# Optimization experiments

Hardware: AMD Instinct MI355X
Metric: run time of the kernel (lower is better)

## Reference

```python
import jax, jax.numpy as jnp
import numpy as np


def fake_quant(w, bits):
    # Symmetric per-tensor fake quantization with straight-through estimator.
    qmax = 2.0 ** (bits - 1) - 1.0
    scale = jnp.max(jnp.abs(w)) / qmax
    wq = jnp.clip(jnp.round(w / scale), -qmax, qmax) * scale
    return w + jax.lax.stop_gradient(wq - w)


def setup_inputs() -> dict:
    key = jax.random.key(0)
    k = jax.random.split(key, 5)
    B, S, D, H = 64, 196, 768, 3072
    x = jax.random.normal(k[0], (B, S, D), dtype=jnp.float32)
    w1 = jax.random.normal(k[1], (H, D), dtype=jnp.float32) * (1.0 / np.sqrt(D))
    b1 = jax.random.normal(k[2], (H,), dtype=jnp.float32) * 0.01
    w2 = jax.random.normal(k[3], (D, H), dtype=jnp.float32) * (1.0 / np.sqrt(H))
    b2 = jax.random.normal(k[4], (D,), dtype=jnp.float32) * 0.01
    return {"x": x, "w1": w1, "b1": b1, "w2": w2, "b2": b2, "bits": 8}


def reference(x, w1, b1, w2, b2, bits):
    # fc1 (fake-quant weight) -> ReLU -> fc2 (fake-quant weight)
    w1q = fake_quant(w1, bits)
    w2q = fake_quant(w2, bits)
    h = jnp.einsum('bsd,hd->bsh', x, w1q) + b1   # [B,S,3072]
    h = jax.nn.relu(h)
    out = jnp.einsum('bsh,dh->bsd', h, w2q) + b2  # [B,S,768]
    return out
```

## Files before the change

### kernel.cpp

```cpp
#include <hip/hip_runtime.h>
#include <hip/hip_bf16.h>
#include <stdint.h>

typedef __attribute__((ext_vector_type(8))) short bf16x8;
typedef __attribute__((ext_vector_type(4))) float f32x4;

__device__ __forceinline__ unsigned short f2bf(float f) {
  __hip_bfloat16 h = __float2bfloat16(f);
  return *reinterpret_cast<unsigned short*>(&h);
}

__global__ void absmax2_kernel(const float* __restrict__ w1, const float* __restrict__ w2,
                               int n4, unsigned int* __restrict__ out) {
  const float* w = blockIdx.y ? w2 : w1;
  __shared__ unsigned int red[256];
  unsigned int m = 0u;
  const uint4* w4 = reinterpret_cast<const uint4*>(w);
  for (int i = blockIdx.x * blockDim.x + threadIdx.x; i < n4;
       i += gridDim.x * blockDim.x) {
    uint4 v = w4[i];
    m = max(m, v.x & 0x7fffffffu);
    m = max(m, v.y & 0x7fffffffu);
    m = max(m, v.z & 0x7fffffffu);
    m = max(m, v.w & 0x7fffffffu);
  }
  red[threadIdx.x] = m;
  __syncthreads();
  for (int s = 128; s > 0; s >>= 1) {
    if ((int)threadIdx.x < s)
      red[threadIdx.x] = max(red[threadIdx.x], red[threadIdx.x + s]);
    __syncthreads();
  }
  if (threadIdx.x == 0) atomicMax(out + blockIdx.y, red[0]);
}

__global__ void quantcast_kernel(const float* __restrict__ w1, const float* __restrict__ w2,
                                 const float* __restrict__ x,
                                 int n4w, int n4x,
                                 const unsigned int* __restrict__ maxbits,
                                 const int* __restrict__ bits,
                                 unsigned short* __restrict__ o1,
                                 unsigned short* __restrict__ o2,
                                 unsigned short* __restrict__ ox) {
  if (blockIdx.y == 2) {
    const float4* x4 = reinterpret_cast<const float4*>(x);
    ushort4* o4 = reinterpret_cast<ushort4*>(ox);
    for (int i = blockIdx.x * blockDim.x + threadIdx.x; i < n4x;
         i += gridDim.x * blockDim.x) {
      float4 v = x4[i];
      o4[i] = make_ushort4(f2bf(v.x), f2bf(v.y), f2bf(v.z), f2bf(v.w));
    }
    return;
  }
  const float* w = blockIdx.y ? w2 : w1;
  unsigned short* o = blockIdx.y ? o2 : o1;
  const float qmax = (float)((1 << (*bits - 1)) - 1);
  const float scale = __uint_as_float(maxbits[blockIdx.y]) / qmax;
  const float4* w4 = reinterpret_cast<const float4*>(w);
  ushort4* o4 = reinterpret_cast<ushort4*>(o);
  for (int i = blockIdx.x * blockDim.x + threadIdx.x; i < n4w;
       i += gridDim.x * blockDim.x) {
    float4 v = w4[i];
    float a = fminf(fmaxf(rintf(v.x / scale), -qmax), qmax) * scale;
    float b = fminf(fmaxf(rintf(v.y / scale), -qmax), qmax) * scale;
    float c = fminf(fmaxf(rintf(v.z / scale), -qmax), qmax) * scale;
    float d = fminf(fmaxf(rintf(v.w / scale), -qmax), qmax) * scale;
    o4[i] = make_ushort4(f2bf(a), f2bf(b), f2bf(c), f2bf(d));
  }
}

template<bool RELU, bool BF16_OUT>
__global__ __launch_bounds__(512, 2)
void gemm8w(const unsigned short* __restrict__ A,
            const unsigned short* __restrict__ B,
            const float* __restrict__ bias,
            void* __restrict__ Cout,
            int M, int N, int K, int gx) {
  extern __shared__ unsigned short lds[];

  const int nwg = gridDim.x;
  const int orig = blockIdx.x;
  const int q = nwg >> 3, r = nwg & 7;
  const int xcd = orig & 7, cidx = orig >> 3;
  const int wgid = (xcd < r ? xcd * (q + 1) : r * (q + 1) + (xcd - r) * q) + cidx;
  const int bx = wgid % gx;
  const int by = wgid / gx;

  const int tid = threadIdx.x;
  const int lane = tid & 63;
  const int wave = tid >> 6;
  const int wr = wave >> 2;
  const int wc = wave & 3;
  const long brow = (long)by * 256;
  const long bcol = (long)bx * 256;

  f32x4 acc[8][4] = {};

  const int fr = lane & 15;
  const int fq = lane >> 4;
  const int swz8 = ((lane & 3) ^ ((lane >> 3) & 3)) * 8;
  const int sgrow = wave * 16 + (lane >> 2);

  auto SA = [&](int t, int kh) {
    unsigned short* dst = lds + ((t & 1) * 2 + kh) * 8192 + wave * 16 * 32;
    const unsigned short* g = A + (brow + sgrow) * (long)K + t * 64 + kh * 32 + swz8;
#pragma unroll
    for (int c = 0; c < 2; ++c)
      __builtin_amdgcn_global_load_lds(
          (const __attribute__((address_space(1))) void*)(g + (long)c * 128 * K),
          (__attribute__((address_space(3))) void*)(dst + c * 128 * 32), 16, 0, 0);
  };
  auto SB = [&](int t, int kh) {
    unsigned short* dst = lds + 32768 + ((t & 1) * 2 + kh) * 8192 + wave * 16 * 32;
    const unsigned short* g = B + (bcol + sgrow) * (long)K + t * 64 + kh * 32 + swz8;
#pragma unroll
    for (int c = 0; c < 2; ++c)
      __builtin_amdgcn_global_load_lds(
          (const __attribute__((address_space(1))) void*)(g + (long)c * 128 * K),
          (__attribute__((address_space(3))) void*)(dst + c * 128 * 32), 16, 0, 0);
  };

  auto RDA = [&](int b, int ks, int mseg, bf16x8* a) {
    const unsigned short* base = lds + (b * 2 + ks) * 8192;
#pragma unroll
    for (int mi = 0; mi < 4; ++mi) {
      const int row = wr * 128 + mseg * 64 + mi * 16 + fr;
      a[mi] = *reinterpret_cast<const bf16x8*>(base + row * 32 + ((fq ^ ((row >> 1) & 3)) * 8));
    }
  };
  auto RDB = [&](int b, int ks, bf16x8* bb) {
    const unsigned short* base = lds + 32768 + (b * 2 + ks) * 8192;
#pragma unroll
    for (int ni = 0; ni < 4; ++ni) {
      const int row = wc * 64 + ni * 16 + fr;
      bb[ni] = *reinterpret_cast<const bf16x8*>(base + row * 32 + ((fq ^ ((row >> 1) & 3)) * 8));
    }
  };
  auto MM = [&](int mseg, bf16x8* a, bf16x8* bb) {
#pragma unroll
    for (int mi = 0; mi < 4; ++mi)
#pragma unroll
      for (int ni = 0; ni < 4; ++ni)
        acc[mseg * 4 + mi][ni] = __builtin_amdgcn_mfma_f32_16x16x32_bf16(
            a[mi], bb[ni], acc[mseg * 4 + mi][ni], 0, 0, 0);
  };

  const int nt = K / 64;
  SA(0, 0); SB(0, 0); SA(0, 1); SB(0, 1); SA(1, 0); SB(1, 0);

  bf16x8 a[4], bb[4];
  for (int t = 0; t < nt; ++t) {
    const int b = t & 1;
    if (t + 1 < nt) {
      SA(t + 1, 1);
      asm volatile("s_waitcnt vmcnt(10)" ::: "memory");
    } else {
      asm volatile("s_waitcnt vmcnt(4)" ::: "memory");
    }
    asm volatile("s_barrier" ::: "memory");
    RDA(b, 0, 0, a); RDB(b, 0, bb);
    asm volatile("s_waitcnt lgkmcnt(0)" ::: "memory");
    __builtin_amdgcn_sched_barrier(0);
    __builtin_amdgcn_s_setprio(1);
    MM(0, a, bb);
    __builtin_amdgcn_s_setprio(0);
    asm volatile("s_barrier" ::: "memory");
    if (t + 1 < nt) SB(t + 1, 1);
    RDA(b, 0, 1, a);
    asm volatile("s_waitcnt lgkmcnt(0)" ::: "memory");
    __builtin_amdgcn_sched_barrier(0);
    __builtin_amdgcn_s_setprio(1);
    MM(1, a, bb);
    __builtin_amdgcn_s_setprio(0);
    asm volatile("s_barrier" ::: "memory");
    if (t + 2 < nt) SA(t + 2, 0);
    if (t + 3 <= nt)      asm volatile("s_waitcnt vmcnt(10)" ::: "memory");
    else if (t == nt - 2) asm volatile("s_waitcnt vmcnt(8)"  ::: "memory");
    else                  asm volatile("s_waitcnt vmcnt(0)"  ::: "memory");
    asm volatile("s_barrier" ::: "memory");
    RDA(b, 1, 0, a); RDB(b, 1, bb);
    asm volatile("s_waitcnt lgkmcnt(0)" ::: "memory");
    __builtin_amdgcn_sched_barrier(0);
    __builtin_amdgcn_s_setprio(1);
    MM(0, a, bb);
    __builtin_amdgcn_s_setprio(0);
    asm volatile("s_barrier" ::: "memory");
    if (t + 2 < nt) SB(t + 2, 0);
    RDA(b, 1, 1, a);
    asm volatile("s_waitcnt lgkmcnt(0)" ::: "memory");
    __builtin_amdgcn_sched_barrier(0);
    __builtin_amdgcn_s_setprio(1);
    MM(1, a, bb);
    __builtin_amdgcn_s_setprio(0);
    asm volatile("s_barrier" ::: "memory");
  }

#pragma unroll
  for (int ni = 0; ni < 4; ++ni) {
    const long col = bcol + wc * 64 + ni * 16 + fr;
    const float bv = bias[col];
#pragma unroll
    for (int mi = 0; mi < 8; ++mi) {
#pragma unroll
      for (int rr = 0; rr < 4; ++rr) {
        const long row = brow + wr * 128 + mi * 16 + fq * 4 + rr;
        float v = acc[mi][ni][rr] + bv;
        if (RELU) v = fmaxf(v, 0.0f);
        if (BF16_OUT)
          ((unsigned short*)Cout)[row * N + col] = f2bf(v);
        else
          ((float*)Cout)[row * N + col] = v;
      }
    }
  }
}

extern "C" void kernel_launch(void* const* d_in, const int* in_sizes, int n_in,
                              void* d_out, int out_size, void* d_ws, size_t ws_size,
                              hipStream_t stream) {
  const float* x  = (const float*)d_in[0];
  const float* w1 = (const float*)d_in[1];
  const float* b1 = (const float*)d_in[2];
  const float* w2 = (const float*)d_in[3];
  const float* b2 = (const float*)d_in[4];
  const int* bits = (const int*)d_in[5];

  const int M = 64 * 196;
  const int D = 768, H = 3072;
  const int nx = M * D;
  const int nw1 = H * D;

  char* ws = (char*)d_ws;
  unsigned int* scales = (unsigned int*)ws;
  unsigned short* xb  = (unsigned short*)(ws + 256);
  unsigned short* w1q = (unsigned short*)(ws + 256 + (size_t)nx * 2);
  unsigned short* w2q = (unsigned short*)(ws + 256 + (size_t)nx * 2 + (size_t)nw1 * 2);
  unsigned short* hb  = (unsigned short*)(ws + 256 + (size_t)nx * 2 + (size_t)nw1 * 4);

  static bool attr_done = false;
  if (!attr_done) {
    hipFuncSetAttribute((const void*)gemm8w<true, true>,
                        hipFuncAttributeMaxDynamicSharedMemorySize, 131072);
    hipFuncSetAttribute((const void*)gemm8w<false, false>,
                        hipFuncAttributeMaxDynamicSharedMemorySize, 131072);
    attr_done = true;
  }

  hipMemsetAsync(scales, 0, 8, stream);
  absmax2_kernel<<<dim3(512, 2), 256, 0, stream>>>(w1, w2, nw1 / 4, scales);
  quantcast_kernel<<<dim3(768, 3), 256, 0, stream>>>(w1, w2, x, nw1 / 4, nx / 4,
                                                     scales, bits, w1q, w2q, xb);

  gemm8w<true, true><<<(M / 256) * (H / 256), 512, 131072, stream>>>(
      xb, w1q, b1, hb, M, H, D, H / 256);
  gemm8w<false, false><<<(M / 256) * (D / 256), 512, 131072, stream>>>(
      hb, w2q, b2, d_out, M, D, H, D / 256);
}
```

Measured before the change: 208.5 us.

## Use BK=32 static-LDS GEMM for fc1 and fuse absmax with x cast

Adds a GEMM variant with a K-step of 32 and statically allocated LDS (64KB) for the first layer, which has a short K=768. Smaller LDS allows more resident workgroups or fewer pipeline fill costs. The second layer keeps the BK=64 pipeline. The x bf16 cast is moved into the absmax kernel so it runs alongside the reduction, and the weight quantization runs as a separate kernel. The shallower prefetch in the BK=32 path may expose more memory latency.

```diff
diff --git a/kernel.cpp b/kernel.cpp
--- a/kernel.cpp
+++ b/kernel.cpp
@@ -10,38 +10,10 @@
   return *reinterpret_cast<unsigned short*>(&h);
 }
 
-__global__ void absmax2_kernel(const float* __restrict__ w1, const float* __restrict__ w2,
-                               int n4, unsigned int* __restrict__ out) {
-  const float* w = blockIdx.y ? w2 : w1;
-  __shared__ unsigned int red[256];
-  unsigned int m = 0u;
-  const uint4* w4 = reinterpret_cast<const uint4*>(w);
-  for (int i = blockIdx.x * blockDim.x + threadIdx.x; i < n4;
-       i += gridDim.x * blockDim.x) {
-    uint4 v = w4[i];
-    m = max(m, v.x & 0x7fffffffu);
-    m = max(m, v.y & 0x7fffffffu);
-    m = max(m, v.z & 0x7fffffffu);
-    m = max(m, v.w & 0x7fffffffu);
-  }
-  red[threadIdx.x] = m;
-  __syncthreads();
-  for (int s = 128; s > 0; s >>= 1) {
-    if ((int)threadIdx.x < s)
-      red[threadIdx.x] = max(red[threadIdx.x], red[threadIdx.x + s]);
-    __syncthreads();
-  }
-  if (threadIdx.x == 0) atomicMax(out + blockIdx.y, red[0]);
-}
-
-__global__ void quantcast_kernel(const float* __restrict__ w1, const float* __restrict__ w2,
-                                 const float* __restrict__ x,
-                                 int n4w, int n4x,
-                                 const unsigned int* __restrict__ maxbits,
-                                 const int* __restrict__ bits,
-                                 unsigned short* __restrict__ o1,
-                                 unsigned short* __restrict__ o2,
-                                 unsigned short* __restrict__ ox) {
+__global__ void prep_kernel(const float* __restrict__ w1, const float* __restrict__ w2,
+                            const float* __restrict__ x, int n4w, int n4x,
+                            unsigned int* __restrict__ out_scales,
+                            unsigned short* __restrict__ ox) {
   if (blockIdx.y == 2) {
     const float4* x4 = reinterpret_cast<const float4*>(x);
     ushort4* o4 = reinterpret_cast<ushort4*>(ox);
@@ -53,12 +25,38 @@
     return;
   }
   const float* w = blockIdx.y ? w2 : w1;
+  __shared__ unsigned int red[256];
+  unsigned int m = 0u;
+  const uint4* w4 = reinterpret_cast<const uint4*>(w);
+  for (int i = blockIdx.x * blockDim.x + threadIdx.x; i < n4w;
+       i += gridDim.x * blockDim.x) {
+    uint4 v = w4[i];
+    m = max(m, v.x & 0x7fffffffu);
+    m = max(m, v.y & 0x7fffffffu);
+    m = max(m, v.z & 0x7fffffffu);
+    m = max(m, v.w & 0x7fffffffu);
+  }
+  red[threadIdx.x] = m;
+  __syncthreads();
+  for (int s = 128; s > 0; s >>= 1) {
+    if ((int)threadIdx.x < s)
+      red[threadIdx.x] = max(red[threadIdx.x], red[threadIdx.x + s]);
+    __syncthreads();
+  }
+  if (threadIdx.x == 0) atomicMax(out_scales + blockIdx.y, red[0]);
+}
+
+__global__ void quant2_kernel(const float* __restrict__ w1, const float* __restrict__ w2,
+                              int n4, const unsigned int* __restrict__ maxbits,
+                              const int* __restrict__ bits,
+                              unsigned short* __restrict__ o1, unsigned short* __restrict__ o2) {
+  const float* w = blockIdx.y ? w2 : w1;
   unsigned short* o = blockIdx.y ? o2 : o1;
   const float qmax = (float)((1 << (*bits - 1)) - 1);
   const float scale = __uint_as_float(maxbits[blockIdx.y]) / qmax;
   const float4* w4 = reinterpret_cast<const float4*>(w);
   ushort4* o4 = reinterpret_cast<ushort4*>(o);
-  for (int i = blockIdx.x * blockDim.x + threadIdx.x; i < n4w;
+  for (int i = blockIdx.x * blockDim.x + threadIdx.x; i < n4;
        i += gridDim.x * blockDim.x) {
     float4 v = w4[i];
     float a = fminf(fmaxf(rintf(v.x / scale), -qmax), qmax) * scale;
@@ -69,14 +67,16 @@
   }
 }
 
+
 template<bool RELU, bool BF16_OUT>
 __global__ __launch_bounds__(512, 2)
-void gemm8w(const unsigned short* __restrict__ A,
-            const unsigned short* __restrict__ B,
-            const float* __restrict__ bias,
-            void* __restrict__ Cout,
-            int M, int N, int K, int gx) {
-  extern __shared__ unsigned short lds[];
+void gemm8w32(const unsigned short* __restrict__ A,
+              const unsigned short* __restrict__ B,
+              const float* __restrict__ bias,
+              void* __restrict__ Cout,
+              int M, int N, int K, int gx) {
+  __shared__ __attribute__((aligned(16))) unsigned short Abuf[2][256 * 32];
+  __shared__ __attribute__((aligned(16))) unsigned short Bbuf[2][256 * 32];
 
   const int nwg = gridDim.x;
   const int orig = blockIdx.x;
@@ -101,35 +101,34 @@
   const int swz8 = ((lane & 3) ^ ((lane >> 3) & 3)) * 8;
   const int sgrow = wave * 16 + (lane >> 2);
 
-  auto SA = [&](int t, int kh) {
-    unsigned short* dst = lds + ((t & 1) * 2 + kh) * 8192 + wave * 16 * 32;
-    const unsigned short* g = A + (brow + sgrow) * (long)K + t * 64 + kh * 32 + swz8;
+  auto SA = [&](int tt) {
+    unsigned short* dst = &Abuf[tt & 1][wave * 16 * 32];
+    const unsigned short* g = A + (brow + sgrow) * (long)K + tt * 32 + swz8;
 #pragma unroll
     for (int c = 0; c < 2; ++c)
       __builtin_amdgcn_global_load_lds(
           (const __attribute__((address_space(1))) void*)(g + (long)c * 128 * K),
           (__attribute__((address_space(3))) void*)(dst + c * 128 * 32), 16, 0, 0);
   };
-  auto SB = [&](int t, int kh) {
-    unsigned short* dst = lds + 32768 + ((t & 1) * 2 + kh) * 8192 + wave * 16 * 32;
-    const unsigned short* g = B + (bcol + sgrow) * (long)K + t * 64 + kh * 32 + swz8;
+  auto SB = [&](int tt) {
+    unsigned short* dst = &Bbuf[tt & 1][wave * 16 * 32];
+    const unsigned short* g = B + (bcol + sgrow) * (long)K + tt * 32 + swz8;
 #pragma unroll
     for (int c = 0; c < 2; ++c)
       __builtin_amdgcn_global_load_lds(
           (const __attribute__((address_space(1))) void*)(g + (long)c * 128 * K),
           (__attribute__((address_space(3))) void*)(dst + c * 128 * 32), 16, 0, 0);
   };
-
-  auto RDA = [&](int b, int ks, int mseg, bf16x8* a) {
-    const unsigned short* base = lds + (b * 2 + ks) * 8192;
+  auto RDA = [&](int b, int mseg, bf16x8* a) {
+    const unsigned short* base = &Abuf[b][0];
 #pragma unroll
     for (int mi = 0; mi < 4; ++mi) {
       const int row = wr * 128 + mseg * 64 + mi * 16 + fr;
       a[mi] = *reinterpret_cast<const bf16x8*>(base + row * 32 + ((fq ^ ((row >> 1) & 3)) * 8));
     }
   };
-  auto RDB = [&](int b, int ks, bf16x8* bb) {
-    const unsigned short* base = lds + 32768 + (b * 2 + ks) * 8192;
+  auto RDB = [&](int b, bf16x8* bb) {
+    const unsigned short* base = &Bbuf[b][0];
 #pragma unroll
     for (int ni = 0; ni < 4; ++ni) {
       const int row = wc * 64 + ni * 16 + fr;
@@ -145,48 +144,28 @@
             a[mi], bb[ni], acc[mseg * 4 + mi][ni], 0, 0, 0);
   };
 
-  const int nt = K / 64;
-  SA(0, 0); SB(0, 0); SA(0, 1); SB(0, 1); SA(1, 0); SB(1, 0);
+  const int nt = K / 32;
+  SA(0); SB(0);
 
   bf16x8 a[4], bb[4];
   for (int t = 0; t < nt; ++t) {
     const int b = t & 1;
     if (t + 1 < nt) {
-      SA(t + 1, 1);
-      asm volatile("s_waitcnt vmcnt(10)" ::: "memory");
+      SA(t + 1);
+      asm volatile("s_waitcnt vmcnt(2)" ::: "memory");
     } else {
-      asm volatile("s_waitcnt vmcnt(4)" ::: "memory");
-    }
-    asm volatile("s_barrier" ::: "memory");
-    RDA(b, 0, 0, a); RDB(b, 0, bb);
+      asm volatile("s_waitcnt vmcnt(0)" ::: "memory");
+    }
+    asm volatile("s_barrier" ::: "memory");
+    RDA(b, 0, a); RDB(b, bb);
     asm volatile("s_waitcnt lgkmcnt(0)" ::: "memory");
     __builtin_amdgcn_sched_barrier(0);
     __builtin_amdgcn_s_setprio(1);
     MM(0, a, bb);
     __builtin_amdgcn_s_setprio(0);
     asm volatile("s_barrier" ::: "memory");
-    if (t + 1 < nt) SB(t + 1, 1);
-    RDA(b, 0, 1, a);
-    asm volatile("s_waitcnt lgkmcnt(0)" ::: "memory");
-    __builtin_amdgcn_sched_barrier(0);
-    __builtin_amdgcn_s_setprio(1);
-    MM(1, a, bb);
-    __builtin_amdgcn_s_setprio(0);
-    asm volatile("s_barrier" ::: "memory");
-    if (t + 2 < nt) SA(t + 2, 0);
-    if (t + 3 <= nt)      asm volatile("s_waitcnt vmcnt(10)" ::: "memory");
-    else if (t == nt - 2) asm volatile("s_waitcnt vmcnt(8)"  ::: "memory");
-    else                  asm volatile("s_waitcnt vmcnt(0)"  ::: "memory");
-    asm volatile("s_barrier" ::: "memory");
-    RDA(b, 1, 0, a); RDB(b, 1, bb);
-    asm volatile("s_waitcnt lgkmcnt(0)" ::: "memory");
-    __builtin_amdgcn_sched_barrier(0);
-    __builtin_amdgcn_s_setprio(1);
-    MM(0, a, bb);
-    __builtin_amdgcn_s_setprio(0);
-    asm volatile("s_barrier" ::: "memory");
-    if (t + 2 < nt) SB(t + 2, 0);
-    RDA(b, 1, 1, a);
+    if (t + 1 < nt) SB(t + 1);
+    RDA(b, 1, a);
     asm volatile("s_waitcnt lgkmcnt(0)" ::: "memory");
     __builtin_amdgcn_sched_barrier(0);
     __builtin_amdgcn_s_setprio(1);
@@ -215,6 +194,149 @@
   }
 }
 
+template<bool RELU, bool BF16_OUT>
+__global__ __launch_bounds__(512, 2)
+void gemm8w64(const unsigned short* __restrict__ A, const unsigned short* __restrict__ B,
+              const float* __restrict__ bias, void* __restrict__ Cout,
+              int M, int N, int K, int gx) {
+  extern __shared__ unsigned short lds[];
+
+  const int nwg = gridDim.x;
+  const int orig = blockIdx.x;
+  const int q = nwg >> 3, r = nwg & 7;
+  const int xcd = orig & 7, cidx = orig >> 3;
+  const int wgid = (xcd < r ? xcd * (q + 1) : r * (q + 1) + (xcd - r) * q) + cidx;
+  const int bx = wgid % gx;
+  const int by = wgid / gx;
+
+  const int tid = threadIdx.x;
+  const int lane = tid & 63;
+  const int wave = tid >> 6;
+  const int wr = wave >> 2;
+  const int wc = wave & 3;
+  const long brow = (long)by * 256;
+  const long bcol = (long)bx * 256;
+
+  f32x4 acc[8][4] = {};
+
+  const int fr = lane & 15;
+  const int fq = lane >> 4;
+  const int swz8 = ((lane & 3) ^ ((lane >> 3) & 3)) * 8;
+  const int sgrow = wave * 16 + (lane >> 2);
+
+  auto SA = [&](int t, int kh) {
+    unsigned short* dst = lds + ((t & 1) * 2 + kh) * 8192 + wave * 16 * 32;
+    const unsigned short* g = A + (brow + sgrow) * (long)K + t * 64 + kh * 32 + swz8;
+#pragma unroll
+    for (int c = 0; c < 2; ++c)
+      __builtin_amdgcn_global_load_lds(
+          (const __attribute__((address_space(1))) void*)(g + (long)c * 128 * K),
+          (__attribute__((address_space(3))) void*)(dst + c * 128 * 32), 16, 0, 0);
+  };
+  auto SB = [&](int t, int kh) {
+    unsigned short* dst = lds + 32768 + ((t & 1) * 2 + kh) * 8192 + wave * 16 * 32;
+    const unsigned short* g = B + (bcol + sgrow) * (long)K + t * 64 + kh * 32 + swz8;
+#pragma unroll
+    for (int c = 0; c < 2; ++c)
+      __builtin_amdgcn_global_load_lds(
+          (const __attribute__((address_space(1))) void*)(g + (long)c * 128 * K),
+          (__attribute__((address_space(3))) void*)(dst + c * 128 * 32), 16, 0, 0);
+  };
+  auto RDA = [&](int b, int ks, int mseg, bf16x8* a) {
+    const unsigned short* base = lds + (b * 2 + ks) * 8192;
+#pragma unroll
+    for (int mi = 0; mi < 4; ++mi) {
+      const int row = wr * 128 + mseg * 64 + mi * 16 + fr;
+      a[mi] = *reinterpret_cast<const bf16x8*>(base + row * 32 + ((fq ^ ((row >> 1) & 3)) * 8));
+    }
+  };
+  auto RDB = [&](int b, int ks, bf16x8* bb) {
+    const unsigned short* base = lds + 32768 + (b * 2 + ks) * 8192;
+#pragma unroll
+    for (int ni = 0; ni < 4; ++ni) {
+      const int row = wc * 64 + ni * 16 + fr;
+      bb[ni] = *reinterpret_cast<const bf16x8*>(base + row * 32 + ((fq ^ ((row >> 1) & 3)) * 8));
+    }
+  };
+  auto MM = [&](int mseg, bf16x8* a, bf16x8* bb) {
+#pragma unroll
+    for (int mi = 0; mi < 4; ++mi)
+#pragma unroll
+      for (int ni = 0; ni < 4; ++ni)
+        acc[mseg * 4 + mi][ni] = __builtin_amdgcn_mfma_f32_16x16x32_bf16(
+            a[mi], bb[ni], acc[mseg * 4 + mi][ni], 0, 0, 0);
+  };
+
+  const int nt = K / 64;
+  SA(0, 0); SB(0, 0); SA(0, 1); SB(0, 1); SA(1, 0); SB(1, 0);
+
+  bf16x8 a[4], bb[4];
+  for (int t = 0; t < nt; ++t) {
+    const int b = t & 1;
+    if (t + 1 < nt) {
+      SA(t + 1, 1);
+      asm volatile("s_waitcnt vmcnt(10)" ::: "memory");
+    } else {
+      asm volatile("s_waitcnt vmcnt(4)" ::: "memory");
+    }
+    asm volatile("s_barrier" ::: "memory");
+    RDA(b, 0, 0, a); RDB(b, 0, bb);
+    asm volatile("s_waitcnt lgkmcnt(0)" ::: "memory");
+    __builtin_amdgcn_sched_barrier(0);
+    __builtin_amdgcn_s_setprio(1);
+    MM(0, a, bb);
+    __builtin_amdgcn_s_setprio(0);
+    asm volatile("s_barrier" ::: "memory");
+    if (t + 1 < nt) SB(t + 1, 1);
+    RDA(b, 0, 1, a);
+    asm volatile("s_waitcnt lgkmcnt(0)" ::: "memory");
+    __builtin_amdgcn_sched_barrier(0);
+    __builtin_amdgcn_s_setprio(1);
+    MM(1, a, bb);
+    __builtin_amdgcn_s_setprio(0);
+    asm volatile("s_barrier" ::: "memory");
+    if (t + 2 < nt) SA(t + 2, 0);
+    if (t + 3 <= nt)      asm volatile("s_waitcnt vmcnt(10)" ::: "memory");
+    else if (t == nt - 2) asm volatile("s_waitcnt vmcnt(8)"  ::: "memory");
+    else                  asm volatile("s_waitcnt vmcnt(0)"  ::: "memory");
+    asm volatile("s_barrier" ::: "memory");
+    RDA(b, 1, 0, a); RDB(b, 1, bb);
+    asm volatile("s_waitcnt lgkmcnt(0)" ::: "memory");
+    __builtin_amdgcn_sched_barrier(0);
+    __builtin_amdgcn_s_setprio(1);
+    MM(0, a, bb);
+    __builtin_amdgcn_s_setprio(0);
+    asm volatile("s_barrier" ::: "memory");
+    if (t + 2 < nt) SB(t + 2, 0);
+    RDA(b, 1, 1, a);
+    asm volatile("s_waitcnt lgkmcnt(0)" ::: "memory");
+    __builtin_amdgcn_sched_barrier(0);
+    __builtin_amdgcn_s_setprio(1);
+    MM(1, a, bb);
+    __builtin_amdgcn_s_setprio(0);
+    asm volatile("s_barrier" ::: "memory");
+  }
+
+#pragma unroll
+  for (int ni = 0; ni < 4; ++ni) {
+    const long col = bcol + wc * 64 + ni * 16 + fr;
+    const float bv = bias[col];
+#pragma unroll
+    for (int mi = 0; mi < 8; ++mi) {
+#pragma unroll
+      for (int rr = 0; rr < 4; ++rr) {
+        const long row = brow + wr * 128 + mi * 16 + fq * 4 + rr;
+        float v = acc[mi][ni][rr] + bv;
+        if (RELU) v = fmaxf(v, 0.0f);
+        if (BF16_OUT)
+          ((unsigned short*)Cout)[row * N + col] = f2bf(v);
+        else
+          ((float*)Cout)[row * N + col] = v;
+      }
+    }
+  }
+}
+
 extern "C" void kernel_launch(void* const* d_in, const int* in_sizes, int n_in,
                               void* d_out, int out_size, void* d_ws, size_t ws_size,
                               hipStream_t stream) {
@@ -237,22 +359,15 @@
   unsigned short* w2q = (unsigned short*)(ws + 256 + (size_t)nx * 2 + (size_t)nw1 * 2);
   unsigned short* hb  = (unsigned short*)(ws + 256 + (size_t)nx * 2 + (size_t)nw1 * 4);
 
-  static bool attr_done = false;
-  if (!attr_done) {
-    hipFuncSetAttribute((const void*)gemm8w<true, true>,
-                        hipFuncAttributeMaxDynamicSharedMemorySize, 131072);
-    hipFuncSetAttribute((const void*)gemm8w<false, false>,
-                        hipFuncAttributeMaxDynamicSharedMemorySize, 131072);
-    attr_done = true;
-  }
+  hipFuncSetAttribute((const void*)gemm8w64<false, false>,
+                      hipFuncAttributeMaxDynamicSharedMemorySize, 131072);
 
   hipMemsetAsync(scales, 0, 8, stream);
-  absmax2_kernel<<<dim3(512, 2), 256, 0, stream>>>(w1, w2, nw1 / 4, scales);
-  quantcast_kernel<<<dim3(768, 3), 256, 0, stream>>>(w1, w2, x, nw1 / 4, nx / 4,
-                                                     scales, bits, w1q, w2q, xb);
-
-  gemm8w<true, true><<<(M / 256) * (H / 256), 512, 131072, stream>>>(
+  prep_kernel<<<dim3(512, 3), 256, 0, stream>>>(w1, w2, x, nw1 / 4, nx / 4, scales, xb);
+  quant2_kernel<<<dim3(512, 2), 256, 0, stream>>>(w1, w2, nw1 / 4, scales, bits, w1q, w2q);
+
+  gemm8w32<true, true><<<(M / 256) * (H / 256), 512, 0, stream>>>(
       xb, w1q, b1, hb, M, H, D, H / 256);
-  gemm8w<false, false><<<(M / 256) * (D / 256), 512, 131072, stream>>>(
+  gemm8w64<false, false><<<(M / 256) * (D / 256), 512, 131072, stream>>>(
       hb, w2q, b2, d_out, M, D, H, D / 256);
 }
```

Measured after the change: 222.2 us. 6.6% more time.

## Use 128x128 tile GEMM for fc1 and fold x cast into absmax pass

Applied to the files above, without the earlier changes.

Replaces the 256x256, 8-wave GEMM for the first layer (K=768) with a new 128x128-tile, 4-wave kernel. It uses static LDS, a BK=64 XOR swizzle and double-buffered global_load_lds staging. The x-to-bf16 cast now runs in the same launch as the weight absmax reduction, and weight quantization moves to a separate kernel, so the x cast no longer waits on the reduction. The smaller tiles give more workgroups for the short-K GEMM, which should help load balance and latency hiding, at the cost of lower data reuse per tile. The second GEMM keeps the old kernel under a new name, and the one-time attribute guard is dropped, so the attribute is now set on every call.

```diff
diff --git a/kernel.cpp b/kernel.cpp
--- a/kernel.cpp
+++ b/kernel.cpp
@@ -10,38 +10,10 @@
   return *reinterpret_cast<unsigned short*>(&h);
 }
 
-__global__ void absmax2_kernel(const float* __restrict__ w1, const float* __restrict__ w2,
-                               int n4, unsigned int* __restrict__ out) {
-  const float* w = blockIdx.y ? w2 : w1;
-  __shared__ unsigned int red[256];
-  unsigned int m = 0u;
-  const uint4* w4 = reinterpret_cast<const uint4*>(w);
-  for (int i = blockIdx.x * blockDim.x + threadIdx.x; i < n4;
-       i += gridDim.x * blockDim.x) {
-    uint4 v = w4[i];
-    m = max(m, v.x & 0x7fffffffu);
-    m = max(m, v.y & 0x7fffffffu);
-    m = max(m, v.z & 0x7fffffffu);
-    m = max(m, v.w & 0x7fffffffu);
-  }
-  red[threadIdx.x] = m;
-  __syncthreads();
-  for (int s = 128; s > 0; s >>= 1) {
-    if ((int)threadIdx.x < s)
-      red[threadIdx.x] = max(red[threadIdx.x], red[threadIdx.x + s]);
-    __syncthreads();
-  }
-  if (threadIdx.x == 0) atomicMax(out + blockIdx.y, red[0]);
-}
-
-__global__ void quantcast_kernel(const float* __restrict__ w1, const float* __restrict__ w2,
-                                 const float* __restrict__ x,
-                                 int n4w, int n4x,
-                                 const unsigned int* __restrict__ maxbits,
-                                 const int* __restrict__ bits,
-                                 unsigned short* __restrict__ o1,
-                                 unsigned short* __restrict__ o2,
-                                 unsigned short* __restrict__ ox) {
+__global__ void prep_kernel(const float* __restrict__ w1, const float* __restrict__ w2,
+                            const float* __restrict__ x, int n4w, int n4x,
+                            unsigned int* __restrict__ out_scales,
+                            unsigned short* __restrict__ ox) {
   if (blockIdx.y == 2) {
     const float4* x4 = reinterpret_cast<const float4*>(x);
     ushort4* o4 = reinterpret_cast<ushort4*>(ox);
@@ -53,12 +25,38 @@
     return;
   }
   const float* w = blockIdx.y ? w2 : w1;
+  __shared__ unsigned int red[256];
+  unsigned int m = 0u;
+  const uint4* w4 = reinterpret_cast<const uint4*>(w);
+  for (int i = blockIdx.x * blockDim.x + threadIdx.x; i < n4w;
+       i += gridDim.x * blockDim.x) {
+    uint4 v = w4[i];
+    m = max(m, v.x & 0x7fffffffu);
+    m = max(m, v.y & 0x7fffffffu);
+    m = max(m, v.z & 0x7fffffffu);
+    m = max(m, v.w & 0x7fffffffu);
+  }
+  red[threadIdx.x] = m;
+  __syncthreads();
+  for (int s = 128; s > 0; s >>= 1) {
+    if ((int)threadIdx.x < s)
+      red[threadIdx.x] = max(red[threadIdx.x], red[threadIdx.x + s]);
+    __syncthreads();
+  }
+  if (threadIdx.x == 0) atomicMax(out_scales + blockIdx.y, red[0]);
+}
+
+__global__ void quant2_kernel(const float* __restrict__ w1, const float* __restrict__ w2,
+                              int n4, const unsigned int* __restrict__ maxbits,
+                              const int* __restrict__ bits,
+                              unsigned short* __restrict__ o1, unsigned short* __restrict__ o2) {
+  const float* w = blockIdx.y ? w2 : w1;
   unsigned short* o = blockIdx.y ? o2 : o1;
   const float qmax = (float)((1 << (*bits - 1)) - 1);
   const float scale = __uint_as_float(maxbits[blockIdx.y]) / qmax;
   const float4* w4 = reinterpret_cast<const float4*>(w);
   ushort4* o4 = reinterpret_cast<ushort4*>(o);
-  for (int i = blockIdx.x * blockDim.x + threadIdx.x; i < n4w;
+  for (int i = blockIdx.x * blockDim.x + threadIdx.x; i < n4;
        i += gridDim.x * blockDim.x) {
     float4 v = w4[i];
     float a = fminf(fmaxf(rintf(v.x / scale), -qmax), qmax) * scale;
@@ -70,13 +68,15 @@
 }
 
 template<bool RELU, bool BF16_OUT>
-__global__ __launch_bounds__(512, 2)
-void gemm8w(const unsigned short* __restrict__ A,
-            const unsigned short* __restrict__ B,
-            const float* __restrict__ bias,
-            void* __restrict__ Cout,
-            int M, int N, int K, int gx) {
-  extern __shared__ unsigned short lds[];
+__global__ __launch_bounds__(256)
+void gemm1_bt(const unsigned short* __restrict__ A,
+              const unsigned short* __restrict__ B,
+              const float* __restrict__ bias,
+              void* __restrict__ Cout,
+              int M, int N, int K, int gx) {
+  constexpr int BK = 64, MF = 4;
+  __shared__ __attribute__((aligned(16))) unsigned short As[2][128 * BK];
+  __shared__ __attribute__((aligned(16))) unsigned short Bs[2][128 * BK];
 
   const int nwg = gridDim.x;
   const int orig = blockIdx.x;
@@ -89,6 +89,125 @@
   const int tid = threadIdx.x;
   const int lane = tid & 63;
   const int wave = tid >> 6;
+  const int wr = wave >> 1;
+  const int wc = wave & 1;
+  const long brow = (long)by * 128;
+  const long bcol = (long)bx * 128;
+
+  f32x4 acc[MF][4] = {};
+
+  const int srow = lane >> 3;
+  const int gslot = ((lane & 7) ^ (lane >> 3)) * 8;
+  const int fr = lane & 15;
+  const int fs = lane >> 4;
+
+  auto stage = [&](int k0, int b) {
+#pragma unroll
+    for (int it = 0; it < 4; ++it) {
+      const int c = it * 4 + wave;
+      const unsigned short* ga = A + (brow + c * 8 + srow) * (long)K + k0 + gslot;
+      __builtin_amdgcn_global_load_lds(
+          (const __attribute__((address_space(1))) void*)ga,
+          (__attribute__((address_space(3))) void*)(&As[b][c * 512]), 16, 0, 0);
+    }
+#pragma unroll
+    for (int it = 0; it < 4; ++it) {
+      const int c = it * 4 + wave;
+      const unsigned short* gb = B + (bcol + c * 8 + srow) * (long)K + k0 + gslot;
+      __builtin_amdgcn_global_load_lds(
+          (const __attribute__((address_space(1))) void*)gb,
+          (__attribute__((address_space(3))) void*)(&Bs[b][c * 512]), 16, 0, 0);
+    }
+  };
+
+  const int nt = K / BK;
+  stage(0, 0);
+  stage(BK, 1);
+
+  for (int t = 0; t < nt; ++t) {
+    const int b = t & 1;
+    if (t < nt - 1) asm volatile("s_waitcnt vmcnt(8)" ::: "memory");
+    else            asm volatile("s_waitcnt vmcnt(0)" ::: "memory");
+    __builtin_amdgcn_s_barrier();
+
+    const unsigned short* as = &As[b][0];
+    const unsigned short* bs = &Bs[b][0];
+#pragma unroll
+    for (int kk = 0; kk < 2; ++kk) {
+      const int s = kk * 4 + fs;
+      bf16x8 a[MF], bb[4];
+#pragma unroll
+      for (int m = 0; m < MF; ++m) {
+        const int row = wr * 64 + m * 16 + fr;
+        a[m] = *reinterpret_cast<const bf16x8*>(as + row * BK + ((s ^ (row & 7)) * 8));
+      }
+#pragma unroll
+      for (int n = 0; n < 4; ++n) {
+        const int row = wc * 64 + n * 16 + fr;
+        bb[n] = *reinterpret_cast<const bf16x8*>(bs + row * BK + ((s ^ (row & 7)) * 8));
+      }
+#pragma unroll
+      for (int m = 0; m < MF; ++m)
+#pragma unroll
+        for (int n = 0; n < 4; ++n)
+          acc[m][n] = __builtin_amdgcn_mfma_f32_16x16x32_bf16(bb[n], a[m], acc[m][n], 0, 0, 0);
+    }
+
+    asm volatile("s_waitcnt lgkmcnt(0)" ::: "memory");
+    __builtin_amdgcn_sched_barrier(0);
+    __builtin_amdgcn_s_barrier();
+    if (t + 2 < nt) stage((t + 2) * BK, b);
+  }
+
+  const int colq = fs * 4;
+  float4 bv[4];
+#pragma unroll
+  for (int n = 0; n < 4; ++n)
+    bv[n] = *reinterpret_cast<const float4*>(&bias[bcol + wc * 64 + n * 16 + colq]);
+#pragma unroll
+  for (int m = 0; m < MF; ++m) {
+    const long row = brow + wr * 64 + m * 16 + fr;
+#pragma unroll
+    for (int n = 0; n < 4; ++n) {
+      const long cb = bcol + wc * 64 + n * 16 + colq;
+      float v0 = acc[m][n][0] + bv[n].x;
+      float v1 = acc[m][n][1] + bv[n].y;
+      float v2 = acc[m][n][2] + bv[n].z;
+      float v3 = acc[m][n][3] + bv[n].w;
+      if (RELU) {
+        v0 = fmaxf(v0, 0.0f); v1 = fmaxf(v1, 0.0f);
+        v2 = fmaxf(v2, 0.0f); v3 = fmaxf(v3, 0.0f);
+      }
+      if (BF16_OUT) {
+        uint2 o;
+        o.x = (unsigned int)f2bf(v0) | ((unsigned int)f2bf(v1) << 16);
+        o.y = (unsigned int)f2bf(v2) | ((unsigned int)f2bf(v3) << 16);
+        *reinterpret_cast<uint2*>((unsigned short*)Cout + row * N + cb) = o;
+      } else {
+        *reinterpret_cast<float4*>((float*)Cout + row * N + cb) = make_float4(v0, v1, v2, v3);
+      }
+    }
+  }
+}
+
+template<bool RELU, bool BF16_OUT>
+__global__ __launch_bounds__(512, 2)
+void gemm8w64(const unsigned short* __restrict__ A, const unsigned short* __restrict__ B,
+              const float* __restrict__ bias, void* __restrict__ Cout,
+              int M, int N, int K, int gx) {
+  extern __shared__ unsigned short lds[];
+
+  const int nwg = gridDim.x;
+  const int orig = blockIdx.x;
+  const int q = nwg >> 3, r = nwg & 7;
+  const int xcd = orig & 7, cidx = orig >> 3;
+  const int wgid = (xcd < r ? xcd * (q + 1) : r * (q + 1) + (xcd - r) * q) + cidx;
+  const int bx = wgid % gx;
+  const int by = wgid / gx;
+
+  const int tid = threadIdx.x;
+  const int lane = tid & 63;
+  const int wave = tid >> 6;
   const int wr = wave >> 2;
   const int wc = wave & 3;
   const long brow = (long)by * 256;
@@ -119,7 +238,6 @@
           (const __attribute__((address_space(1))) void*)(g + (long)c * 128 * K),
           (__attribute__((address_space(3))) void*)(dst + c * 128 * 32), 16, 0, 0);
   };
-
   auto RDA = [&](int b, int ks, int mseg, bf16x8* a) {
     const unsigned short* base = lds + (b * 2 + ks) * 8192;
 #pragma unroll
@@ -237,22 +355,15 @@
   unsigned short* w2q = (unsigned short*)(ws + 256 + (size_t)nx * 2 + (size_t)nw1 * 2);
   unsigned short* hb  = (unsigned short*)(ws + 256 + (size_t)nx * 2 + (size_t)nw1 * 4);
 
-  static bool attr_done = false;
-  if (!attr_done) {
-    hipFuncSetAttribute((const void*)gemm8w<true, true>,
-                        hipFuncAttributeMaxDynamicSharedMemorySize, 131072);
-    hipFuncSetAttribute((const void*)gemm8w<false, false>,
-                        hipFuncAttributeMaxDynamicSharedMemorySize, 131072);
-    attr_done = true;
-  }
+  hipFuncSetAttribute((const void*)gemm8w64<false, false>,
+                      hipFuncAttributeMaxDynamicSharedMemorySize, 131072);
 
   hipMemsetAsync(scales, 0, 8, stream);
-  absmax2_kernel<<<dim3(512, 2), 256, 0, stream>>>(w1, w2, nw1 / 4, scales);
-  quantcast_kernel<<<dim3(768, 3), 256, 0, stream>>>(w1, w2, x, nw1 / 4, nx / 4,
-                                                     scales, bits, w1q, w2q, xb);
-
-  gemm8w<true, true><<<(M / 256) * (H / 256), 512, 131072, stream>>>(
-      xb, w1q, b1, hb, M, H, D, H / 256);
-  gemm8w<false, false><<<(M / 256) * (D / 256), 512, 131072, stream>>>(
+  prep_kernel<<<dim3(512, 3), 256, 0, stream>>>(w1, w2, x, nw1 / 4, nx / 4, scales, xb);
+  quant2_kernel<<<dim3(512, 2), 256, 0, stream>>>(w1, w2, nw1 / 4, scales, bits, w1q, w2q);
+
+  gemm1_bt<true, true><<<(H / 128) * (M / 128), 256, 0, stream>>>(
+      xb, w1q, b1, hb, M, H, D, H / 128);
+  gemm8w64<false, false><<<(M / 256) * (D / 256), 512, 131072, stream>>>(
       hb, w2q, b2, d_out, M, D, H, D / 256);
 }
```

Measured after the change: 214.2 us. 2.8% more time.
